# Kernel optimization log

Measured on AMD Instinct MI355X. Metric: run time of the kernel, lower is better.

Reference implementation:

```python
import jax, jax.numpy as jnp
import numpy as np

# Module hyperparameters (BNMorph.__init__ defaults + KITTI resolution)
B, H, W = 8, 320, 1024
SEARCH_W = 7      # serachWidth
SEARCH_H = 3      # searchHeight
SPARSITY_RAD = 2
SENSE_R = 20
PIX_DW = 24.0     # pixel_distance_weight
ALPHA_DW = 0.7    # alpha_distance_weight
PIX_MUL_DW = 1.9  # pixel_mulline_distance_weight
ALPHA_PAD = 1.6   # alpha_padding
EDGE_DENSITY = 0.02


def _make_offsets():
    # Exactly mirrors BNMorph.__init__ buffer construction.
    rs = np.arange(-SEARCH_W, SEARCH_W + 1)
    cs = np.arange(-SEARCH_H, SEARCH_H + 1)
    xx, yy = np.meshgrid(rs, cs)
    xx = xx.flatten(); yy = yy.flatten()
    idx = np.argsort(xx ** 2 + yy ** 2)
    xx = xx[idx]; yy = yy[idx]
    ss = np.arange(-SPARSITY_RAD, SPARSITY_RAD + 1)
    sxx, syy = np.meshgrid(ss, ss)
    sxx = sxx.flatten(); syy = syy.flatten()
    cspan = np.arange(-SENSE_R, SENSE_R + 1)
    cxx, cyy = np.meshgrid(cspan, cspan)
    cxx = cxx.flatten(); cyy = cyy.flatten()
    ci = np.argsort(cxx ** 2 + cyy ** 2)
    cxx = cxx[ci]; cyy = cyy[ci]
    f32 = lambda a: jnp.asarray(a, dtype=jnp.float32)
    return f32(xx), f32(yy), f32(sxx), f32(syy), f32(cxx), f32(cyy)


def setup_inputs() -> dict:
    key = jax.random.key(0)
    k1, k2 = jax.random.split(key)
    binMapsrc = (jax.random.uniform(k1, (B, 1, H, W)) < EDGE_DENSITY).astype(jnp.float32)
    binMapdst = (jax.random.uniform(k2, (B, 1, H, W)) < EDGE_DENSITY).astype(jnp.float32)
    xx, yy, sxx, syy, cxx, cyy = _make_offsets()
    return {"binMapsrc": binMapsrc, "binMapdst": binMapdst,
            "xx": xx, "yy": yy, "sxx": sxx, "syy": syy, "cxx": cxx, "cyy": cyy}


def _forward(binMapsrc, binMapdst, xx, yy, sxx, syy, cxx, cyy):
    src = binMapsrc[:, 0] > 0.5  # [B,H,W] bool
    dst = binMapdst[:, 0] > 0.5
    b, h, w = src.shape

    # ---- 1. sparsity filtering of src edge points ----
    # keep an active pixel iff no active pixel precedes it (raster order)
    # inside the sparsity window -> approximates greedy sparsification.
    sdx = sxx.astype(jnp.int32); sdy = syy.astype(jnp.int32)
    prec = ((sdy < 0) | ((sdy == 0) & (sdx < 0))).astype(jnp.float32)
    Ps = jnp.pad(src.astype(jnp.float32),
                 ((0, 0), (SPARSITY_RAD, SPARSITY_RAD), (SPARSITY_RAD, SPARSITY_RAD)))

    def sp_step(acc, off):
        dx, dy, wk = off
        sl = jax.lax.dynamic_slice(Ps, (0, SPARSITY_RAD + dy, SPARSITY_RAD + dx), (b, h, w))
        return acc + sl * wk, None

    acc, _ = jax.lax.scan(sp_step, jnp.zeros((b, h, w), jnp.float32), (sdx, sdy, prec))
    kept = src & (acc < 0.5)

    # ---- 2. windowed nearest-correspondence search in dst ----
    # offsets (xx,yy) are pre-sorted by distance, so the first hit is nearest.
    qdx = xx.astype(jnp.int32); qdy = yy.astype(jnp.int32)
    Pd = jnp.pad(dst, ((0, 0), (SEARCH_H, SEARCH_H), (SEARCH_W, SEARCH_W)))

    def m_step(carry, off):
        found, vx, vy = carry
        dx, dy, dxf, dyf = off
        sl = jax.lax.dynamic_slice(Pd, (0, SEARCH_H + dy, SEARCH_W + dx), (b, h, w))
        hit = sl & kept & (~found)
        vx = jnp.where(hit, dxf, vx)
        vy = jnp.where(hit, dyf, vy)
        return (found | hit, vx, vy), None

    init = (jnp.zeros((b, h, w), bool),
            jnp.zeros((b, h, w), jnp.float32),
            jnp.zeros((b, h, w), jnp.float32))
    (found, vx, vy), _ = jax.lax.scan(m_step, init, (qdx, qdy, xx, yy))

    # ---- 3. distance-weighted morph field (splat = depthwise conv) ----
    d = jnp.sqrt(cxx ** 2 + cyy ** 2)
    wts = ALPHA_DW * jnp.exp(-d * PIX_MUL_DW / PIX_DW)
    R = SENSE_R
    K = jnp.zeros((2 * R + 1, 2 * R + 1), jnp.float32)
    K = K.at[cyy.astype(jnp.int32) + R, cxx.astype(jnp.int32) + R].set(wts)

    m = found.astype(jnp.float32)
    inp = jnp.stack([m, m * vx, m * vy], axis=1)        # [B,3,H,W]
    ker = jnp.tile(K[None, None], (3, 1, 1, 1))          # [3,1,41,41]
    out = jax.lax.conv_general_dilated(
        inp, ker, (1, 1), ((R, R), (R, R)),
        dimension_numbers=("NCHW", "OIHW", "NCHW"), feature_group_count=3)
    den = out[:, 0] + ALPHA_PAD
    dispx = out[:, 1] / den
    dispy = out[:, 2] / den

    ygrid, xgrid = jnp.meshgrid(jnp.arange(h, dtype=jnp.float32),
                                jnp.arange(w, dtype=jnp.float32), indexing="ij")
    morphedx = xgrid + dispx
    morphedy = ygrid + dispy
    orgpts_x = xgrid * m
    orgpts_y = ygrid * m
    correspts_x = (xgrid + vx) * m
    correspts_y = (ygrid + vy) * m
    return morphedx, morphedy, orgpts_x, orgpts_y, correspts_x, correspts_y


def reference(binMapsrc, binMapdst, xx, yy, sxx, syy, cxx, cyy):
    return _forward(binMapsrc, binMapdst, xx, yy, sxx, syy, cxx, cyy)
```

## Files before the change

### kernel.cpp

```cpp
#include <hip/hip_runtime.h>


#define BB 8
#define HH 320
#define WW 1024
#define N_PIX (BB*HH*WW)
#define WPI (HH*(WW/32))
#define RR 20
#define TLW 64
#define TLH 32
#define TXN (WW/TLW)
#define TYN (HH/TLH)
#define NQ 105
#define CAP 192
#define WTABN (4*42*48)
#define WTAB_OFF (2*BB*WPI*4)

typedef unsigned long long u64;
typedef float v2f __attribute__((ext_vector_type(2)));

__global__ __launch_bounds__(256) void pack_zero(
    const float* __restrict__ src, const float* __restrict__ dst,
    unsigned* __restrict__ packed, float* __restrict__ wtab_g)
{
    int t = threadIdx.x;
    int i = blockIdx.x * 256 + t;
    if (i < WTABN) {
        int rot = i / (42 * 48);
        int rem = i - rot * (42 * 48);
        int row = rem / 48, c = rem - row * 48;
        int pc = c + rot;
        float v = 0.0f;
        if (row <= 40 && pc >= 4 && pc <= 44) {
            int dxv = pc - 24, dyv = row - 20;
            float d = sqrtf((float)(dxv * dxv + dyv * dyv));
            v = 0.7f * expf((-d * 1.9f) / 24.0f);
        }
        wtab_g[i] = v;
    }
    const float4* p = (i < (N_PIX >> 2)) ? (const float4*)src + i
                                         : (const float4*)dst + (i - (N_PIX >> 2));
    float4 v = *p;
    unsigned nib = (v.x > 0.5f ? 1u : 0u) | (v.y > 0.5f ? 2u : 0u)
                 | (v.z > 0.5f ? 4u : 0u) | (v.w > 0.5f ? 8u : 0u);
    unsigned val = nib << ((t & 7) * 4);
    val |= __shfl_xor(val, 1);
    val |= __shfl_xor(val, 2);
    val |= __shfl_xor(val, 4);
    if ((t & 7) == 0) packed[i >> 3] = val;
}

__global__ __launch_bounds__(256, 4) void fused_morph(
    const unsigned* __restrict__ packed,
    const float* __restrict__ xx, const float* __restrict__ yy,
    const float* __restrict__ wtab_g,
    float* __restrict__ out)
{
    __shared__ __align__(16) float wtab[WTABN];
    __shared__ unsigned sSrc[74][6];
    __shared__ unsigned sDst[78][6];
    __shared__ __align__(16) unsigned sPt[CAP];
    __shared__ int prank[NQ];
    __shared__ unsigned char sVB[TLH * TLW];
    __shared__ int lcnt;

    int t = threadIdx.x;
    int txT = blockIdx.x, tyT = blockIdx.y, b = blockIdx.z;
    int tx0 = txT * TLW, ty0 = tyT * TLH;
    int wb0 = (tx0 >> 5) - 1;
    const unsigned* psrc = packed + (size_t)b * WPI;
    const unsigned* pdst = packed + (size_t)(BB + b) * WPI;

    for (int i = t; i < WTABN / 4; i += 256)
        ((float4*)wtab)[i] = ((const float4*)wtab_g)[i];
    for (int i = t; i < 74 * 4; i += 256) {
        int r = i >> 2, w = (i & 3) + 1;
        int gy = ty0 - 22 + r, gw = wb0 + (w - 1);
        sSrc[r][w] = (gy >= 0 && gy < HH && gw >= 0 && gw < 32) ? psrc[(gy << 5) + gw] : 0u;
    }
    for (int i = t; i < 78 * 4; i += 256) {
        int r = i >> 2, w = (i & 3) + 1;
        int gy = ty0 - 23 + r, gw = wb0 + (w - 1);
        sDst[r][w] = (gy >= 0 && gy < HH && gw >= 0 && gw < 32) ? pdst[(gy << 5) + gw] : 0u;
    }
    if (t < 78) { sDst[t][0] = 0; sDst[t][5] = 0; if (t < 74) { sSrc[t][0] = 0; sSrc[t][5] = 0; } }
    if (t < NQ) {
        int dx = (int)xx[t], dy = (int)yy[t];
        prank[(dy + 3) * 15 + (dx + 7)] = (t << 8) | ((dx + 7) << 4) | (dy + 3);
    }
    ((unsigned*)sVB)[t] = 0; ((unsigned*)sVB)[t + 256] = 0;
    if (t == 0) lcnt = 0;
    __syncthreads();

    for (int task = t; task < 288; task += 256) {
        int cr = task >> 2, w = (task & 3) + 1;
        unsigned C = sSrc[cr + 2][w];
        unsigned found = 0;
        if (C) {
            #define EXT5(row) ( (u64)((row)[w-1] >> 30) \
                              | ((u64)(row)[w] << 2) \
                              | ((u64)((row)[w+1] & 3u) << 34) )
            u64 a = EXT5(sSrc[cr]) | EXT5(sSrc[cr + 1]);
            u64 or5 = a | (a >> 1) | (a >> 2) | (a >> 3) | (a >> 4);
            u64 e2 = EXT5(sSrc[cr + 2]);
            unsigned kept = C & ~(unsigned)(or5 | e2 | (e2 >> 1));
            if (kept) {
                u64 dil = 0;
                #pragma unroll
                for (int rr = 0; rr < 7; ++rr) {
                    const unsigned* row = sDst[cr + rr];
                    dil |= (u64)(row[w-1] >> 25) | ((u64)row[w] << 7)
                         | ((u64)(row[w+1] & 0x7Fu) << 39);
                }
                u64 a2 = dil | (dil >> 1);
                u64 b2 = a2 | (a2 >> 2);
                u64 c2 = b2 | (b2 >> 4);
                u64 o15 = c2 | (c2 >> 7);
                found = kept & (unsigned)o15;
            }
        }
        if (w == 1) found &= 0xFFFFF000u;
        if (w == 4) found &= 0x000FFFFFu;
        if (found) {
            int nf = __popc(found);
            int base = atomicAdd(&lcnt, nf);
            unsigned fi = found;
            while (fi) {
                int bit = __builtin_ctz(fi); fi &= fi - 1;
                int px = tx0 - 32 + ((w - 1) << 5) + bit;
                if (base < CAP) sPt[base] = (unsigned)((cr << 10) | px);
                ++base;
            }
        }
    }
    __syncthreads();
    int nPts = lcnt; if (nPts > CAP) nPts = CAP;
    int n4 = (nPts + 3) & ~3;

    if (t < nPts) {
        unsigned e = sPt[t];
        int cr = (int)(e >> 10), px = (int)(e & 1023u);
        int q = px - tx0 + 25;
        int widx = 1 + (q >> 5), sh = q & 31;
        u64 lo = 0, hi = 0;
        #pragma unroll
        for (int rr = 0; rr < 7; ++rr) {
            const unsigned* row = sDst[cr + rr];
            u64 win = (((u64)row[widx] | ((u64)row[widx + 1] << 32)) >> sh) & 0x7FFFull;
            if (rr < 4) lo |= win << (15 * rr);
            else        hi |= win << (15 * (rr - 4));
        }
        int minv = 0x7FFFFFFF;
        while (lo) { int bb2 = __builtin_ctzll(lo); lo &= lo - 1; int rv = prank[bb2];      if (rv < minv) minv = rv; }
        while (hi) { int bb2 = __builtin_ctzll(hi); hi &= hi - 1; int rv = prank[60 + bb2]; if (rv < minv) minv = rv; }
        int vxp7 = (minv >> 4) & 15, vyp3 = minv & 15;
        int py = ty0 - 20 + cr;
        sPt[t] = (unsigned)px | ((unsigned)py << 10)
               | ((unsigned)vxp7 << 19) | ((unsigned)vyp3 << 23);
        if (px >= tx0 && px < tx0 + TLW && cr >= 20 && cr < 20 + TLH)
            sVB[(cr - 20) * TLW + (px - tx0)] =
                (unsigned char)(0x80 | vxp7 | (vyp3 << 4));
    }
    if (t < n4 - nPts) sPt[nPts + t] = 0xFFFFFFFFu;
    __syncthreads();

    int x0q = tx0 + (t & 15) * 4;
    int y0t = ty0 + (t >> 4) * 2;

    v2f a0p[2][2] = {};
    v2f av[2][4]  = {};

    for (int p = 0; p < n4; p += 4) {
        uint4 P = *(const uint4*)&sPt[p];
        #pragma unroll
        for (int k = 0; k < 4; ++k) {
            int spk = __builtin_amdgcn_readfirstlane(
                (int)(k == 0 ? P.x : k == 1 ? P.y : k == 2 ? P.z : P.w));
            int pxp21 = (spk & 1023) + 21;
            int pyp20 = ((spk >> 10) & 511) + 20;
            float pvx = (float)(((spk >> 19) & 15) - 7);
            float pvy = (float)(((spk >> 23) & 7) - 3);
            v2f vv = {pvx, pvy};

            int coff = pxp21 - x0q;
            coff = coff < 0 ? 0 : (coff > 45 ? 45 : coff);
            int rot = coff & 3;
            int cb  = rot * (42 * 48) + (coff & ~3);
            #pragma unroll
            for (int ry = 0; ry < 2; ++ry) {
                int dyr = pyp20 - (y0t + ry);
                int rowi = ((unsigned)dyr > 40u) ? 41 : dyr;
                float4 wv = *(const float4*)&wtab[cb + rowi * 48];
                a0p[ry][0] += (v2f){wv.w, wv.z};
                a0p[ry][1] += (v2f){wv.y, wv.x};
                av[ry][0] += wv.w * vv;
                av[ry][1] += wv.z * vv;
                av[ry][2] += wv.y * vv;
                av[ry][3] += wv.x * vv;
            }
        }
    }

    size_t bbase = (size_t)b * HH * WW;
    int lx = x0q - tx0;
    #pragma unroll
    for (int ry = 0; ry < 2; ++ry) {
        int y = y0t + ry;
        int ly = y - ty0;
        unsigned vb4 = *(const unsigned*)&sVB[ly * TLW + lx];
        size_t idx = bbase + (size_t)y * WW + x0q;
        float d0 = a0p[ry][0].x + 1.6f, d1 = a0p[ry][0].y + 1.6f;
        float d2 = a0p[ry][1].x + 1.6f, d3 = a0p[ry][1].y + 1.6f;
        float4 ox = { (float)x0q     + av[ry][0].x / d0, (float)(x0q+1) + av[ry][1].x / d1,
                      (float)(x0q+2) + av[ry][2].x / d2, (float)(x0q+3) + av[ry][3].x / d3 };
        float4 oy = { (float)y + av[ry][0].y / d0, (float)y + av[ry][1].y / d1,
                      (float)y + av[ry][2].y / d2, (float)y + av[ry][3].y / d3 };
        float4 o2, o3, o4, o5;
        float* po2 = &o2.x; float* po3 = &o3.x; float* po4 = &o4.x; float* po5 = &o5.x;
        #pragma unroll
        for (int jj = 0; jj < 4; ++jj) {
            unsigned by = (vb4 >> (8 * jj)) & 255u;
            float fm  = (float)(by >> 7);
            float fvx = (float)((int)(by & 15u) - 7);
            float fvy = (float)((int)((by >> 4) & 7u) - 3);
            float fx  = (float)(x0q + jj);
            po2[jj] = fx * fm;
            po3[jj] = (float)y * fm;
            po4[jj] = (fx + fvx) * fm;
            po5[jj] = ((float)y + fvy) * fm;
        }
        *reinterpret_cast<float4*>(out + idx)                     = ox;
        *reinterpret_cast<float4*>(out + (size_t)N_PIX + idx)     = oy;
        *reinterpret_cast<float4*>(out + 2 * (size_t)N_PIX + idx) = o2;
        *reinterpret_cast<float4*>(out + 3 * (size_t)N_PIX + idx) = o3;
        *reinterpret_cast<float4*>(out + 4 * (size_t)N_PIX + idx) = o4;
        *reinterpret_cast<float4*>(out + 5 * (size_t)N_PIX + idx) = o5;
    }
}

extern "C" void kernel_launch(void* const* d_in, const int* in_sizes, int n_in,
                              void* d_out, int out_size, void* d_ws, size_t ws_size,
                              hipStream_t stream) {
    const float* src = (const float*)d_in[0];
    const float* dst = (const float*)d_in[1];
    const float* xx  = (const float*)d_in[2];
    const float* yy  = (const float*)d_in[3];
    float* out = (float*)d_out;

    unsigned* packed = (unsigned*)d_ws;
    float*    wtab_g = (float*)((char*)d_ws + WTAB_OFF);

    pack_zero<<<(2 * N_PIX / 4) / 256, 256, 0, stream>>>(src, dst, packed, wtab_g);

    dim3 g2(TXN, TYN, BB);
    fused_morph<<<g2, 256, 0, stream>>>(packed, xx, yy, wtab_g, out);
}
```

Before: 140.1 us.

## Cull splat points per wavefront by row band and shrink weight table

Before accumulating, each wavefront compacts the tile's point list with a ballot into a private list. The list keeps only the points whose kernel footprint can reach that wave's 8-row band, which removes per-point work that contributes nothing. The weight table now has two column rotations at stride 52 instead of four at stride 48 and is read with two 8-byte loads. This roughly halves its LDS footprint and the launch bound asks for 5 blocks per CU instead of 4. The extra compaction pass and per-wave buffer add LDS traffic, and the smaller loads may raise instruction count or bank conflicts.

```diff
diff --git a/kernel.cpp b/kernel.cpp
--- a/kernel.cpp
+++ b/kernel.cpp
@@ -13,7 +13,8 @@
 #define TYN (HH/TLH)
 #define NQ 105
 #define CAP 192
-#define WTABN (4*42*48)
+#define WSTRIDE 52
+#define WTABN (2*42*WSTRIDE)
 #define WTAB_OFF (2*BB*WPI*4)
 
 typedef unsigned long long u64;
@@ -26,9 +27,9 @@
     int t = threadIdx.x;
     int i = blockIdx.x * 256 + t;
     if (i < WTABN) {
-        int rot = i / (42 * 48);
-        int rem = i - rot * (42 * 48);
-        int row = rem / 48, c = rem - row * 48;
+        int rot = i / (42 * WSTRIDE);
+        int rem = i - rot * (42 * WSTRIDE);
+        int row = rem / WSTRIDE, c = rem - row * WSTRIDE;
         int pc = c + rot;
         float v = 0.0f;
         if (row <= 40 && pc >= 4 && pc <= 44) {
@@ -50,7 +51,7 @@
     if ((t & 7) == 0) packed[i >> 3] = val;
 }
 
-__global__ __launch_bounds__(256, 4) void fused_morph(
+__global__ __launch_bounds__(256, 5) void fused_morph(
     const unsigned* __restrict__ packed,
     const float* __restrict__ xx, const float* __restrict__ yy,
     const float* __restrict__ wtab_g,
@@ -60,6 +61,7 @@
     __shared__ unsigned sSrc[74][6];
     __shared__ unsigned sDst[78][6];
     __shared__ __align__(16) unsigned sPt[CAP];
+    __shared__ __align__(16) unsigned sWav[4][200];
     __shared__ int prank[NQ];
     __shared__ unsigned char sVB[TLH * TLW];
     __shared__ int lcnt;
@@ -135,7 +137,6 @@
     }
     __syncthreads();
     int nPts = lcnt; if (nPts > CAP) nPts = CAP;
-    int n4 = (nPts + 3) & ~3;
 
     if (t < nPts) {
         unsigned e = sPt[t];
@@ -161,8 +162,25 @@
             sVB[(cr - 20) * TLW + (px - tx0)] =
                 (unsigned char)(0x80 | vxp7 | (vyp3 << 4));
     }
-    if (t < n4 - nPts) sPt[nPts + t] = 0xFFFFFFFFu;
     __syncthreads();
+
+    int lane = t & 63, w = __builtin_amdgcn_readfirstlane(t >> 6);
+    int wy0 = ty0 + w * 8;
+    int cw = 0;
+    for (int base = 0; base < nPts; base += 64) {
+        int i = base + lane;
+        unsigned pk = (i < nPts) ? sPt[i] : 0xFFFFFFFFu;
+        int py = (int)((pk >> 10) & 511u);
+        bool pass = (i < nPts) & (py >= wy0 - 20) & (py <= wy0 + 27);
+        u64 m = __ballot(pass);
+        if (pass) {
+            int idx = __popcll(m & ((1ull << lane) - 1ull));
+            sWav[w][cw + idx] = pk;
+        }
+        cw += __popcll(m);
+    }
+    int c4 = (cw + 3) & ~3;
+    if (lane < c4 - cw) sWav[w][cw + lane] = 0xFFFFFFFFu;
 
     int x0q = tx0 + (t & 15) * 4;
     int y0t = ty0 + (t >> 4) * 2;
@@ -170,8 +188,8 @@
     v2f a0p[2][2] = {};
     v2f av[2][4]  = {};
 
-    for (int p = 0; p < n4; p += 4) {
-        uint4 P = *(const uint4*)&sPt[p];
+    for (int p = 0; p < c4; p += 4) {
+        uint4 P = *(const uint4*)&sWav[w][p];
         #pragma unroll
         for (int k = 0; k < 4; ++k) {
             int spk = __builtin_amdgcn_readfirstlane(
@@ -184,19 +202,21 @@
 
             int coff = pxp21 - x0q;
             coff = coff < 0 ? 0 : (coff > 45 ? 45 : coff);
-            int rot = coff & 3;
-            int cb  = rot * (42 * 48) + (coff & ~3);
+            int rot = coff & 1;
+            int cb  = rot * (42 * WSTRIDE) + (coff & ~1);
             #pragma unroll
             for (int ry = 0; ry < 2; ++ry) {
                 int dyr = pyp20 - (y0t + ry);
                 int rowi = ((unsigned)dyr > 40u) ? 41 : dyr;
-                float4 wv = *(const float4*)&wtab[cb + rowi * 48];
-                a0p[ry][0] += (v2f){wv.w, wv.z};
-                a0p[ry][1] += (v2f){wv.y, wv.x};
-                av[ry][0] += wv.w * vv;
-                av[ry][1] += wv.z * vv;
-                av[ry][2] += wv.y * vv;
-                av[ry][3] += wv.x * vv;
+                const float* wr = &wtab[cb + rowi * WSTRIDE];
+                v2f w01 = *(const v2f*)wr;
+                v2f w23 = *(const v2f*)(wr + 2);
+                a0p[ry][0] += (v2f){w23.y, w23.x};
+                a0p[ry][1] += (v2f){w01.y, w01.x};
+                av[ry][0] += w23.y * vv;
+                av[ry][1] += w23.x * vv;
+                av[ry][2] += w01.y * vv;
+                av[ry][3] += w01.x * vv;
             }
         }
     }
```

After: 124.6 us. -11.1%, faster.
